# Kernel tuning notes

Hardware: AMD Instinct MI355X
Metric: run time of the kernel (lower is better)

Reference implementation:

```python
import jax, jax.numpy as jnp
import numpy as np

B, T, C = 64, 4096, 256
H = 4
HD = C // H  # head_dim = 64
EPS = 1e-5   # torch LayerNorm default


def setup_inputs() -> dict:
    key = jax.random.key(0)
    ks = jax.random.split(key, 8)
    x = jax.random.normal(ks[0], (B, T, C), dtype=jnp.float32)
    # per-head score MLP: Linear(C->HD) + Tanh + Linear(HD->1, no bias)
    W1 = jax.random.normal(ks[1], (H, C, HD), dtype=jnp.float32) * (1.0 / np.sqrt(C))
    b1 = jax.random.normal(ks[2], (H, HD), dtype=jnp.float32) * 0.02
    w2 = jax.random.normal(ks[3], (H, HD), dtype=jnp.float32) * (1.0 / np.sqrt(HD))
    # output projection Linear(H*C -> C), torch layout (out, in)
    Wo = jax.random.normal(ks[4], (C, H * C), dtype=jnp.float32) * (1.0 / np.sqrt(H * C))
    bo = jax.random.normal(ks[5], (C,), dtype=jnp.float32) * 0.02
    gamma = jnp.ones((C,), dtype=jnp.float32)
    beta = jnp.zeros((C,), dtype=jnp.float32)
    return {"x": x, "W1": W1, "b1": b1, "w2": w2, "Wo": Wo, "bo": bo,
            "gamma": gamma, "beta": beta}


def reference(x, W1, b1, w2, Wo, bo, gamma, beta):
    # All heads batched: hidden (B,H,T,HD)
    h = jnp.tanh(jnp.einsum('btc,hcd->bhtd', x, W1) + b1[None, :, None, :])
    scores = jnp.einsum('bhtd,hd->bht', h, w2)            # (B,H,T)
    weights = jax.nn.softmax(scores, axis=-1)             # softmax over T
    contexts = jnp.einsum('bht,btc->bhc', weights, x)     # (B,H,C)
    multi = contexts.reshape(B, H * C)                    # concat over heads
    out = multi @ Wo.T + bo                               # Linear(H*C->C)
    # LayerNorm over last dim (dropout is identity in eval mode)
    mu = jnp.mean(out, axis=-1, keepdims=True)
    var = jnp.mean(jnp.square(out - mu), axis=-1, keepdims=True)
    out = (out - mu) * jax.lax.rsqrt(var + EPS) * gamma + beta
    return out, weights
```

## Files before the change

### kernel.cpp

```cpp
#include <hip/hip_runtime.h>
#include <hip/hip_bf16.h>
#include <math.h>

#define B_ 64
#define T_ 4096
#define C_ 256
#define H_ 4
#define HD_ 64
#define EPS_ 1e-5f

typedef __attribute__((ext_vector_type(4))) float floatx4;
typedef __attribute__((ext_vector_type(8))) short short8;

#if __has_builtin(__builtin_amdgcn_cvt_pk_bf16_f32)
typedef __attribute__((ext_vector_type(2))) __bf16 bf16x2_t;
__device__ __forceinline__ unsigned int pack_bf16x2(float a, float b) {
    bf16x2_t v = __builtin_amdgcn_cvt_pk_bf16_f32(a, b);
    return __builtin_bit_cast(unsigned int, v);
}
#else
__device__ __forceinline__ unsigned int pack_bf16x2(float a, float b) {
    unsigned int ua = __builtin_bit_cast(unsigned int, a);
    unsigned int ub = __builtin_bit_cast(unsigned int, b);
    ua = (ua + 0x7fffu + ((ua >> 16) & 1u)) >> 16;
    ub = (ub + 0x7fffu + ((ub >> 16) & 1u)) >> 16;
    return ua | (ub << 16);
}
#endif

__device__ __forceinline__ float fast_tanh(float v) {
    float a = fabsf(v);
    float e = __expf(-2.0f * a);
#if __has_builtin(__builtin_amdgcn_rcpf)
    float r = (1.0f - e) * __builtin_amdgcn_rcpf(1.0f + e);
#else
    float r = (1.0f - e) / (1.0f + e);
#endif
    return copysignf(r, v);
}

__global__ void k0_w1frag(const float* __restrict__ W1, uint4* __restrict__ w1f) {
    int h  = blockIdx.x >> 3;
    int ks = blockIdx.x & 7;
    int nb = threadIdx.x >> 6;
    int l  = threadIdx.x & 63;
    int nl = l & 15, q = l >> 4;
    int d  = nb * 16 + nl;
    const float* src = W1 + ((long)h * C_ + ks * 32 + q * 8) * HD_ + d;
    float v[8];
    #pragma unroll
    for (int j = 0; j < 8; ++j) v[j] = src[j * HD_];
    uint4 ua;
    ua.x = pack_bf16x2(v[0], v[1]); ua.y = pack_bf16x2(v[2], v[3]);
    ua.z = pack_bf16x2(v[4], v[5]); ua.w = pack_bf16x2(v[6], v[7]);
    w1f[((long)blockIdx.x * 4 + nb) * 64 + l] = ua;
}

#define ASTRIDE 264
__global__ __launch_bounds__(256, 4)
void k1_fused(const float* __restrict__ x, const uint4* __restrict__ w1f,
              const float* __restrict__ b1, const float* __restrict__ w2,
              float* __restrict__ rawscore, float* __restrict__ ctxp,
              float* __restrict__ mS) {
    __shared__ __align__(16) unsigned short shA[64 * ASTRIDE];
    __shared__ float sS[4 * 64];
    __shared__ __align__(16) float sP4[64 * 4];

    const int tid  = threadIdx.x;
    const int lane = tid & 63;
    const int w    = tid >> 6;
    const int nl   = lane & 15;
    const int q    = lane >> 4;
    const int rowbase = blockIdx.x * 64;
    const int b       = blockIdx.x >> 6;
    const int tbase   = (blockIdx.x & 63) * 64;

    const int arow = tid >> 2;
    const int acol = (tid & 3) * 8;
    const float* aptr = x + (long)(rowbase + arow) * C_ + acol;
    #pragma unroll
    for (int kc = 0; kc < 8; ++kc) {
        const float4* ap = (const float4*)(aptr + kc * 32);
        float4 f0 = ap[0], f1 = ap[1];
        uint4 ua;
        ua.x = pack_bf16x2(f0.x, f0.y); ua.y = pack_bf16x2(f0.z, f0.w);
        ua.z = pack_bf16x2(f1.x, f1.y); ua.w = pack_bf16x2(f1.z, f1.w);
        *(uint4*)&shA[arow * ASTRIDE + kc * 32 + acol] = ua;
    }

    floatx4 acc[4][4];
    #pragma unroll
    for (int i = 0; i < 4; ++i)
        #pragma unroll
        for (int j = 0; j < 4; ++j)
            acc[i][j] = (floatx4){0.f, 0.f, 0.f, 0.f};

    const uint4* bW = w1f + (long)w * (8 * 4 * 64) + lane;

    uint4 bFa[4], bFb[4];
    #pragma unroll
    for (int nb = 0; nb < 4; ++nb) bFa[nb] = bW[nb * 64];

    __syncthreads();

    #pragma unroll
    for (int kp = 0; kp < 4; ++kp) {
        const int ks0 = 2 * kp, ks1 = 2 * kp + 1;
        #pragma unroll
        for (int nb = 0; nb < 4; ++nb) bFb[nb] = bW[(ks1 * 4 + nb) * 64];
        #pragma unroll
        for (int mb = 0; mb < 4; ++mb) {
            short8 a = *(const short8*)&shA[(mb * 16 + nl) * ASTRIDE + ks0 * 32 + q * 8];
            #pragma unroll
            for (int nb = 0; nb < 4; ++nb)
                acc[mb][nb] = __builtin_amdgcn_mfma_f32_16x16x32_bf16(
                    a, __builtin_bit_cast(short8, bFa[nb]), acc[mb][nb], 0, 0, 0);
        }
        if (kp < 3) {
            #pragma unroll
            for (int nb = 0; nb < 4; ++nb) bFa[nb] = bW[((ks0 + 2) * 4 + nb) * 64];
        }
        #pragma unroll
        for (int mb = 0; mb < 4; ++mb) {
            short8 a = *(const short8*)&shA[(mb * 16 + nl) * ASTRIDE + ks1 * 32 + q * 8];
            #pragma unroll
            for (int nb = 0; nb < 4; ++nb)
                acc[mb][nb] = __builtin_amdgcn_mfma_f32_16x16x32_bf16(
                    a, __builtin_bit_cast(short8, bFb[nb]), acc[mb][nb], 0, 0, 0);
        }
    }

    float b1v[4], w2v[4];
    #pragma unroll
    for (int nb = 0; nb < 4; ++nb) {
        int d = nb * 16 + nl;
        b1v[nb] = b1[w * HD_ + d];
        w2v[nb] = w2[w * HD_ + d];
    }
    #pragma unroll
    for (int mb = 0; mb < 4; ++mb) {
        float p[4];
        #pragma unroll
        for (int r = 0; r < 4; ++r) {
            float s = 0.f;
            #pragma unroll
            for (int nb = 0; nb < 4; ++nb)
                s += fast_tanh(acc[mb][nb][r] + b1v[nb]) * w2v[nb];
            p[r] = s;
        }
        #pragma unroll
        for (int m = 1; m < 16; m <<= 1)
            #pragma unroll
            for (int r = 0; r < 4; ++r)
                p[r] += __shfl_xor(p[r], m, 64);
        if (nl == 0) {
            #pragma unroll
            for (int r = 0; r < 4; ++r)
                sS[w * 64 + mb * 16 + q * 4 + r] = p[r];
        }
    }

    {
        float s = sS[w * 64 + lane];
        float m = s;
        #pragma unroll
        for (int off = 1; off < 64; off <<= 1)
            m = fmaxf(m, __shfl_xor(m, off, 64));
        float e = __expf(s - m);
        float Ss = e;
        #pragma unroll
        for (int off = 1; off < 64; off <<= 1)
            Ss += __shfl_xor(Ss, off, 64);
        sP4[lane * 4 + w] = e;
        rawscore[((long)(b * H_ + w)) * T_ + tbase + lane] = s;
        if (lane == 0) {
            mS[((long)blockIdx.x * H_ + w) * 2 + 0] = m;
            mS[((long)blockIdx.x * H_ + w) * 2 + 1] = Ss;
        }
    }
    __syncthreads();

    {
        float c0 = 0.f, c1 = 0.f, c2 = 0.f, c3 = 0.f;
        const float* xr = x + (long)rowbase * C_ + tid;
        const float4* pv4 = (const float4*)sP4;
        #pragma unroll 8
        for (int t = 0; t < 64; ++t) {
            float xv = xr[(long)t * C_];
            float4 pv = pv4[t];
            c0 += pv.x * xv;
            c1 += pv.y * xv;
            c2 += pv.z * xv;
            c3 += pv.w * xv;
        }
        float* o = ctxp + (long)blockIdx.x * (H_ * C_) + tid;
        o[0]   = c0;
        o[256] = c1;
        o[512] = c2;
        o[768] = c3;
    }
}

__global__ void k2_combine(const float* __restrict__ ctxp, const float* __restrict__ mS,
                           float* __restrict__ weights, float* __restrict__ multi) {
    __shared__ float sm[64], sSl[64], sc[64];
    int bh = blockIdx.x;
    int b = bh >> 2, h = bh & 3;
    int tid = threadIdx.x;
    if (tid < 64) {
        long blk = (long)b * 64 + tid;
        sm[tid]  = mS[(blk * H_ + h) * 2 + 0];
        sSl[tid] = mS[(blk * H_ + h) * 2 + 1];
    }
    __syncthreads();
    float m = -INFINITY;
    #pragma unroll 8
    for (int j = 0; j < 64; ++j) m = fmaxf(m, sm[j]);
    if (tid < 64) sc[tid] = __expf(sm[tid] - m);
    __syncthreads();
    float S = 0.f;
    #pragma unroll 8
    for (int j = 0; j < 64; ++j) S += sSl[j] * sc[j];
    float invS = 1.0f / S;

    float acc = 0.f;
    #pragma unroll 4
    for (int j = 0; j < 64; ++j)
        acc += ctxp[((long)(b * 64 + j) * H_ + h) * C_ + tid] * sc[j];
    multi[(long)b * (H_ * C_) + h * C_ + tid] = acc * invS;

    float* wr = weights + (long)bh * T_;
    #pragma unroll
    for (int i = 0; i < 16; ++i) {
        int t = tid + i * 256;
        float sv = wr[t];
        wr[t] = __expf(sv - m) * invS;
    }
}

__global__ void k4_out(const float* __restrict__ multiG, const float* __restrict__ Wo,
                       const float* __restrict__ bo, const float* __restrict__ gamma,
                       const float* __restrict__ beta, float* __restrict__ out) {
    __shared__ float multi[1024];
    __shared__ float red[256];
    int b = blockIdx.x, tid = threadIdx.x;
    {
        const float4* src = (const float4*)(multiG + (long)b * 1024);
        float4* dst = (float4*)multi;
        dst[tid] = src[tid];
    }
    __syncthreads();
    float a0 = 0.f, a1 = 0.f, a2 = 0.f, a3 = 0.f;
    const float4* wrow = (const float4*)(Wo + (long)tid * 1024);
    const float4* mv = (const float4*)multi;
    #pragma unroll 8
    for (int j4 = 0; j4 < 256; j4 += 4) {
        float4 w0 = wrow[j4],     m0 = mv[j4];
        float4 w1 = wrow[j4 + 1], m1 = mv[j4 + 1];
        float4 w2 = wrow[j4 + 2], m2 = mv[j4 + 2];
        float4 w3 = wrow[j4 + 3], m3 = mv[j4 + 3];
        a0 += m0.x * w0.x + m0.y * w0.y + m0.z * w0.z + m0.w * w0.w;
        a1 += m1.x * w1.x + m1.y * w1.y + m1.z * w1.z + m1.w * w1.w;
        a2 += m2.x * w2.x + m2.y * w2.y + m2.z * w2.z + m2.w * w2.w;
        a3 += m3.x * w3.x + m3.y * w3.y + m3.z * w3.z + m3.w * w3.w;
    }
    float acc = bo[tid] + ((a0 + a1) + (a2 + a3));
    red[tid] = acc; __syncthreads();
    for (int st = 128; st > 0; st >>= 1) {
        if (tid < st) red[tid] += red[tid + st];
        __syncthreads();
    }
    float mu = red[0] * (1.0f / 256.0f); __syncthreads();
    float dv = acc - mu;
    red[tid] = dv * dv; __syncthreads();
    for (int st = 128; st > 0; st >>= 1) {
        if (tid < st) red[tid] += red[tid + st];
        __syncthreads();
    }
    float var = red[0] * (1.0f / 256.0f);
    out[(long)b * C_ + tid] = dv * rsqrtf(var + EPS_) * gamma[tid] + beta[tid];
}

extern "C" void kernel_launch(void* const* d_in, const int* in_sizes, int n_in,
                              void* d_out, int out_size, void* d_ws, size_t ws_size,
                              hipStream_t stream) {
    const float* x     = (const float*)d_in[0];
    const float* W1    = (const float*)d_in[1];
    const float* b1    = (const float*)d_in[2];
    const float* w2    = (const float*)d_in[3];
    const float* Wo    = (const float*)d_in[4];
    const float* bo    = (const float*)d_in[5];
    const float* gamma = (const float*)d_in[6];
    const float* beta  = (const float*)d_in[7];

    float* out     = (float*)d_out;
    float* weights = out + B_ * C_;

    float* ctxp  = (float*)d_ws;
    float* mS    = ctxp + (long)4096 * H_ * C_;
    float* multi = mS + (long)4096 * H_ * 2;
    uint4* w1f   = (uint4*)(multi + B_ * H_ * C_);

    k0_w1frag <<<32, 256, 0, stream>>>(W1, w1f);
    k1_fused  <<<4096, 256, 0, stream>>>(x, w1f, b1, w2, weights, ctxp, mS);
    k2_combine<<<256, 256, 0, stream>>>(ctxp, mS, weights, multi);
    k4_out    <<<64, 256, 0, stream>>>(multi, Wo, bo, gamma, beta, out);
}
```

Baseline: 467.2 us.

## Split each head's hidden dim across two waves with 512-thread blocks

Doubles the k1 block to 8 waves. Each head's 64 hidden units are now split across two waves, and their partial scores are summed in shared memory before the softmax. The x staging and the context accumulation are also split across twice as many threads. The aim is more parallelism and latency hiding per block, at the cost of an extra barrier, idle waves during the softmax, and possibly lower occupancy per CU from the larger blocks.

```diff
diff --git a/kernel.cpp b/kernel.cpp
--- a/kernel.cpp
+++ b/kernel.cpp
@@ -57,49 +57,52 @@
 }
 
 #define ASTRIDE 264
-__global__ __launch_bounds__(256, 4)
+__global__ __launch_bounds__(512, 4)
 void k1_fused(const float* __restrict__ x, const uint4* __restrict__ w1f,
               const float* __restrict__ b1, const float* __restrict__ w2,
               float* __restrict__ rawscore, float* __restrict__ ctxp,
               float* __restrict__ mS) {
     __shared__ __align__(16) unsigned short shA[64 * ASTRIDE];
-    __shared__ float sS[4 * 64];
+    __shared__ float sS[2 * 4 * 64];
     __shared__ __align__(16) float sP4[64 * 4];
 
     const int tid  = threadIdx.x;
     const int lane = tid & 63;
-    const int w    = tid >> 6;
+    const int wid  = tid >> 6;
+    const int h    = wid >> 1;
+    const int nh   = wid & 1;
     const int nl   = lane & 15;
     const int q    = lane >> 4;
     const int rowbase = blockIdx.x * 64;
     const int b       = blockIdx.x >> 6;
     const int tbase   = (blockIdx.x & 63) * 64;
 
-    const int arow = tid >> 2;
-    const int acol = (tid & 3) * 8;
-    const float* aptr = x + (long)(rowbase + arow) * C_ + acol;
-    #pragma unroll
-    for (int kc = 0; kc < 8; ++kc) {
-        const float4* ap = (const float4*)(aptr + kc * 32);
-        float4 f0 = ap[0], f1 = ap[1];
-        uint4 ua;
-        ua.x = pack_bf16x2(f0.x, f0.y); ua.y = pack_bf16x2(f0.z, f0.w);
-        ua.z = pack_bf16x2(f1.x, f1.y); ua.w = pack_bf16x2(f1.z, f1.w);
-        *(uint4*)&shA[arow * ASTRIDE + kc * 32 + acol] = ua;
-    }
-
-    floatx4 acc[4][4];
+    {
+        const int arow = tid >> 3;
+        const int acol = (tid & 7) * 32;
+        const float4* ap = (const float4*)(x + (long)(rowbase + arow) * C_ + acol);
+        #pragma unroll
+        for (int i = 0; i < 4; ++i) {
+            float4 f0 = ap[2 * i], f1 = ap[2 * i + 1];
+            uint4 ua;
+            ua.x = pack_bf16x2(f0.x, f0.y); ua.y = pack_bf16x2(f0.z, f0.w);
+            ua.z = pack_bf16x2(f1.x, f1.y); ua.w = pack_bf16x2(f1.z, f1.w);
+            *(uint4*)&shA[arow * ASTRIDE + acol + i * 8] = ua;
+        }
+    }
+
+    floatx4 acc[4][2];
     #pragma unroll
     for (int i = 0; i < 4; ++i)
         #pragma unroll
-        for (int j = 0; j < 4; ++j)
+        for (int j = 0; j < 2; ++j)
             acc[i][j] = (floatx4){0.f, 0.f, 0.f, 0.f};
 
-    const uint4* bW = w1f + (long)w * (8 * 4 * 64) + lane;
-
-    uint4 bFa[4], bFb[4];
-    #pragma unroll
-    for (int nb = 0; nb < 4; ++nb) bFa[nb] = bW[nb * 64];
+    const uint4* bW = w1f + (long)h * (8 * 4 * 64) + lane;
+
+    uint4 bFa[2], bFb[2];
+    #pragma unroll
+    for (int nb2 = 0; nb2 < 2; ++nb2) bFa[nb2] = bW[(nh * 2 + nb2) * 64];
 
     __syncthreads();
 
@@ -107,35 +110,35 @@
     for (int kp = 0; kp < 4; ++kp) {
         const int ks0 = 2 * kp, ks1 = 2 * kp + 1;
         #pragma unroll
-        for (int nb = 0; nb < 4; ++nb) bFb[nb] = bW[(ks1 * 4 + nb) * 64];
+        for (int nb2 = 0; nb2 < 2; ++nb2) bFb[nb2] = bW[(ks1 * 4 + nh * 2 + nb2) * 64];
         #pragma unroll
         for (int mb = 0; mb < 4; ++mb) {
             short8 a = *(const short8*)&shA[(mb * 16 + nl) * ASTRIDE + ks0 * 32 + q * 8];
             #pragma unroll
-            for (int nb = 0; nb < 4; ++nb)
-                acc[mb][nb] = __builtin_amdgcn_mfma_f32_16x16x32_bf16(
-                    a, __builtin_bit_cast(short8, bFa[nb]), acc[mb][nb], 0, 0, 0);
+            for (int nb2 = 0; nb2 < 2; ++nb2)
+                acc[mb][nb2] = __builtin_amdgcn_mfma_f32_16x16x32_bf16(
+                    a, __builtin_bit_cast(short8, bFa[nb2]), acc[mb][nb2], 0, 0, 0);
         }
         if (kp < 3) {
             #pragma unroll
-            for (int nb = 0; nb < 4; ++nb) bFa[nb] = bW[((ks0 + 2) * 4 + nb) * 64];
+            for (int nb2 = 0; nb2 < 2; ++nb2) bFa[nb2] = bW[((ks0 + 2) * 4 + nh * 2 + nb2) * 64];
         }
         #pragma unroll
         for (int mb = 0; mb < 4; ++mb) {
             short8 a = *(const short8*)&shA[(mb * 16 + nl) * ASTRIDE + ks1 * 32 + q * 8];
             #pragma unroll
-            for (int nb = 0; nb < 4; ++nb)
-                acc[mb][nb] = __builtin_amdgcn_mfma_f32_16x16x32_bf16(
-                    a, __builtin_bit_cast(short8, bFb[nb]), acc[mb][nb], 0, 0, 0);
-        }
-    }
-
-    float b1v[4], w2v[4];
-    #pragma unroll
-    for (int nb = 0; nb < 4; ++nb) {
-        int d = nb * 16 + nl;
-        b1v[nb] = b1[w * HD_ + d];
-        w2v[nb] = w2[w * HD_ + d];
+            for (int nb2 = 0; nb2 < 2; ++nb2)
+                acc[mb][nb2] = __builtin_amdgcn_mfma_f32_16x16x32_bf16(
+                    a, __builtin_bit_cast(short8, bFb[nb2]), acc[mb][nb2], 0, 0, 0);
+        }
+    }
+
+    float b1v[2], w2v[2];
+    #pragma unroll
+    for (int nb2 = 0; nb2 < 2; ++nb2) {
+        int d = (nh * 2 + nb2) * 16 + nl;
+        b1v[nb2] = b1[h * HD_ + d];
+        w2v[nb2] = w2[h * HD_ + d];
     }
     #pragma unroll
     for (int mb = 0; mb < 4; ++mb) {
@@ -144,8 +147,8 @@
         for (int r = 0; r < 4; ++r) {
             float s = 0.f;
             #pragma unroll
-            for (int nb = 0; nb < 4; ++nb)
-                s += fast_tanh(acc[mb][nb][r] + b1v[nb]) * w2v[nb];
+            for (int nb2 = 0; nb2 < 2; ++nb2)
+                s += fast_tanh(acc[mb][nb2][r] + b1v[nb2]) * w2v[nb2];
             p[r] = s;
         }
         #pragma unroll
@@ -156,12 +159,14 @@
         if (nl == 0) {
             #pragma unroll
             for (int r = 0; r < 4; ++r)
-                sS[w * 64 + mb * 16 + q * 4 + r] = p[r];
-        }
-    }
-
-    {
-        float s = sS[w * 64 + lane];
+                sS[(nh * 4 + h) * 64 + mb * 16 + q * 4 + r] = p[r];
+        }
+    }
+    __syncthreads();
+
+    if (tid < 256) {
+        const int w = tid >> 6;
+        float s = sS[w * 64 + lane] + sS[(4 + w) * 64 + lane];
         float m = s;
         #pragma unroll
         for (int off = 1; off < 64; off <<= 1)
@@ -181,23 +186,21 @@
     __syncthreads();
 
     {
-        float c0 = 0.f, c1 = 0.f, c2 = 0.f, c3 = 0.f;
-        const float* xr = x + (long)rowbase * C_ + tid;
-        const float4* pv4 = (const float4*)sP4;
+        const int c  = tid & 255;
+        const int th = tid >> 8;
+        float c0 = 0.f, c1 = 0.f;
+        const float* xr = x + (long)rowbase * C_ + c;
+        const float2* pv2 = (const float2*)sP4;
         #pragma unroll 8
         for (int t = 0; t < 64; ++t) {
             float xv = xr[(long)t * C_];
-            float4 pv = pv4[t];
+            float2 pv = pv2[t * 2 + th];
             c0 += pv.x * xv;
             c1 += pv.y * xv;
-            c2 += pv.z * xv;
-            c3 += pv.w * xv;
-        }
-        float* o = ctxp + (long)blockIdx.x * (H_ * C_) + tid;
+        }
+        float* o = ctxp + (long)blockIdx.x * (H_ * C_) + th * 512 + c;
         o[0]   = c0;
         o[256] = c1;
-        o[512] = c2;
-        o[768] = c3;
     }
 }
 
@@ -302,7 +305,7 @@
     uint4* w1f   = (uint4*)(multi + B_ * H_ * C_);
 
     k0_w1frag <<<32, 256, 0, stream>>>(W1, w1f);
-    k1_fused  <<<4096, 256, 0, stream>>>(x, w1f, b1, w2, weights, ctxp, mS);
+    k1_fused  <<<4096, 512, 0, stream>>>(x, w1f, b1, w2, weights, ctxp, mS);
     k2_combine<<<256, 256, 0, stream>>>(ctxp, mS, weights, multi);
     k4_out    <<<64, 256, 0, stream>>>(multi, Wo, bo, gamma, beta, out);
 }
```

Measured after the change: 478.6 us. +2.4%, slower.

## Halve k1 row tile to 32, double block count, simplify tanh

Applied to the files above, without the earlier changes.

The fused score/context kernel now processes 32 timesteps per block instead of 64, which doubles the grid to 8192 blocks and raises the occupancy hint to 5 blocks per CU. The combine kernel is adjusted to merge 128 partial blocks per batch. The x staging load is rewritten as row-contiguous float4 reads. tanh becomes a sign-free exp2/rcp form. In exchange, each W1 fragment loaded per block now feeds half as many rows, and the partial-context buffer that k1 writes and k2 reads is twice as large.

```diff
diff --git a/kernel.cpp b/kernel.cpp
--- a/kernel.cpp
+++ b/kernel.cpp
@@ -8,6 +8,9 @@
 #define H_ 4
 #define HD_ 64
 #define EPS_ 1e-5f
+
+#define TILE_ 32
+#define NBLK_ 128
 
 typedef __attribute__((ext_vector_type(4))) float floatx4;
 typedef __attribute__((ext_vector_type(8))) short short8;
@@ -29,14 +32,17 @@
 #endif
 
 __device__ __forceinline__ float fast_tanh(float v) {
-    float a = fabsf(v);
-    float e = __expf(-2.0f * a);
+    float t = v * 2.8853900817779268f;
+#if __has_builtin(__builtin_amdgcn_exp2f)
+    float e2 = __builtin_amdgcn_exp2f(t);
+#else
+    float e2 = exp2f(t);
+#endif
 #if __has_builtin(__builtin_amdgcn_rcpf)
-    float r = (1.0f - e) * __builtin_amdgcn_rcpf(1.0f + e);
+    return fmaf(-2.0f, __builtin_amdgcn_rcpf(e2 + 1.0f), 1.0f);
 #else
-    float r = (1.0f - e) / (1.0f + e);
+    return 1.0f - 2.0f / (e2 + 1.0f);
 #endif
-    return copysignf(r, v);
 }
 
 __global__ void k0_w1frag(const float* __restrict__ W1, uint4* __restrict__ w1f) {
@@ -57,40 +63,40 @@
 }
 
 #define ASTRIDE 264
-__global__ __launch_bounds__(256, 4)
+__global__ __launch_bounds__(256, 5)
 void k1_fused(const float* __restrict__ x, const uint4* __restrict__ w1f,
               const float* __restrict__ b1, const float* __restrict__ w2,
               float* __restrict__ rawscore, float* __restrict__ ctxp,
               float* __restrict__ mS) {
-    __shared__ __align__(16) unsigned short shA[64 * ASTRIDE];
-    __shared__ float sS[4 * 64];
-    __shared__ __align__(16) float sP4[64 * 4];
+    __shared__ __align__(16) unsigned short shA[TILE_ * ASTRIDE];
+    __shared__ float sS[4 * TILE_];
+    __shared__ __align__(16) float sP4[TILE_ * 4];
 
     const int tid  = threadIdx.x;
     const int lane = tid & 63;
     const int w    = tid >> 6;
     const int nl   = lane & 15;
     const int q    = lane >> 4;
-    const int rowbase = blockIdx.x * 64;
-    const int b       = blockIdx.x >> 6;
-    const int tbase   = (blockIdx.x & 63) * 64;
-
-    const int arow = tid >> 2;
-    const int acol = (tid & 3) * 8;
-    const float* aptr = x + (long)(rowbase + arow) * C_ + acol;
-    #pragma unroll
-    for (int kc = 0; kc < 8; ++kc) {
-        const float4* ap = (const float4*)(aptr + kc * 32);
-        float4 f0 = ap[0], f1 = ap[1];
-        uint4 ua;
-        ua.x = pack_bf16x2(f0.x, f0.y); ua.y = pack_bf16x2(f0.z, f0.w);
-        ua.z = pack_bf16x2(f1.x, f1.y); ua.w = pack_bf16x2(f1.z, f1.w);
-        *(uint4*)&shA[arow * ASTRIDE + kc * 32 + acol] = ua;
-    }
-
-    floatx4 acc[4][4];
-    #pragma unroll
-    for (int i = 0; i < 4; ++i)
+    const int rowbase = blockIdx.x * TILE_;
+    const int b       = blockIdx.x >> 7;
+    const int tbase   = (blockIdx.x & 127) * TILE_;
+
+    {
+        const int r0 = w * 8;
+        const float* xp = x + (long)(rowbase + r0) * C_ + lane * 4;
+        #pragma unroll
+        for (int i = 0; i < 8; ++i) {
+            float4 f = *(const float4*)(xp + (long)i * C_);
+            uint2 u;
+            u.x = pack_bf16x2(f.x, f.y);
+            u.y = pack_bf16x2(f.z, f.w);
+            *(uint2*)&shA[(r0 + i) * ASTRIDE + lane * 4] = u;
+        }
+    }
+
+    floatx4 acc[2][4];
+    #pragma unroll
+    for (int i = 0; i < 2; ++i)
         #pragma unroll
         for (int j = 0; j < 4; ++j)
             acc[i][j] = (floatx4){0.f, 0.f, 0.f, 0.f};
@@ -109,7 +115,7 @@
         #pragma unroll
         for (int nb = 0; nb < 4; ++nb) bFb[nb] = bW[(ks1 * 4 + nb) * 64];
         #pragma unroll
-        for (int mb = 0; mb < 4; ++mb) {
+        for (int mb = 0; mb < 2; ++mb) {
             short8 a = *(const short8*)&shA[(mb * 16 + nl) * ASTRIDE + ks0 * 32 + q * 8];
             #pragma unroll
             for (int nb = 0; nb < 4; ++nb)
@@ -121,7 +127,7 @@
             for (int nb = 0; nb < 4; ++nb) bFa[nb] = bW[((ks0 + 2) * 4 + nb) * 64];
         }
         #pragma unroll
-        for (int mb = 0; mb < 4; ++mb) {
+        for (int mb = 0; mb < 2; ++mb) {
             short8 a = *(const short8*)&shA[(mb * 16 + nl) * ASTRIDE + ks1 * 32 + q * 8];
             #pragma unroll
             for (int nb = 0; nb < 4; ++nb)
@@ -138,7 +144,7 @@
         w2v[nb] = w2[w * HD_ + d];
     }
     #pragma unroll
-    for (int mb = 0; mb < 4; ++mb) {
+    for (int mb = 0; mb < 2; ++mb) {
         float p[4];
         #pragma unroll
         for (int r = 0; r < 4; ++r) {
@@ -156,26 +162,29 @@
         if (nl == 0) {
             #pragma unroll
             for (int r = 0; r < 4; ++r)
-                sS[w * 64 + mb * 16 + q * 4 + r] = p[r];
-        }
-    }
-
-    {
-        float s = sS[w * 64 + lane];
+                sS[w * TILE_ + mb * 16 + q * 4 + r] = p[r];
+        }
+    }
+    __syncthreads();
+
+    if (tid < 128) {
+        const int wh = tid >> 5;
+        const int tl = tid & 31;
+        float s = sS[wh * TILE_ + tl];
         float m = s;
         #pragma unroll
-        for (int off = 1; off < 64; off <<= 1)
-            m = fmaxf(m, __shfl_xor(m, off, 64));
+        for (int off = 1; off < 32; off <<= 1)
+            m = fmaxf(m, __shfl_xor(m, off, 32));
         float e = __expf(s - m);
         float Ss = e;
         #pragma unroll
-        for (int off = 1; off < 64; off <<= 1)
-            Ss += __shfl_xor(Ss, off, 64);
-        sP4[lane * 4 + w] = e;
-        rawscore[((long)(b * H_ + w)) * T_ + tbase + lane] = s;
-        if (lane == 0) {
-            mS[((long)blockIdx.x * H_ + w) * 2 + 0] = m;
-            mS[((long)blockIdx.x * H_ + w) * 2 + 1] = Ss;
+        for (int off = 1; off < 32; off <<= 1)
+            Ss += __shfl_xor(Ss, off, 32);
+        sP4[tl * 4 + wh] = e;
+        rawscore[((long)(b * H_ + wh)) * T_ + tbase + tl] = s;
+        if (tl == 0) {
+            mS[((long)blockIdx.x * H_ + wh) * 2 + 0] = m;
+            mS[((long)blockIdx.x * H_ + wh) * 2 + 1] = Ss;
         }
     }
     __syncthreads();
@@ -185,7 +194,7 @@
         const float* xr = x + (long)rowbase * C_ + tid;
         const float4* pv4 = (const float4*)sP4;
         #pragma unroll 8
-        for (int t = 0; t < 64; ++t) {
+        for (int t = 0; t < TILE_; ++t) {
             float xv = xr[(long)t * C_];
             float4 pv = pv4[t];
             c0 += pv.x * xv;
@@ -203,30 +212,30 @@
 
 __global__ void k2_combine(const float* __restrict__ ctxp, const float* __restrict__ mS,
                            float* __restrict__ weights, float* __restrict__ multi) {
-    __shared__ float sm[64], sSl[64], sc[64];
+    __shared__ float sm[NBLK_], sSl[NBLK_], sc[NBLK_];
     int bh = blockIdx.x;
     int b = bh >> 2, h = bh & 3;
     int tid = threadIdx.x;
-    if (tid < 64) {
-        long blk = (long)b * 64 + tid;
+    if (tid < NBLK_) {
+        long blk = (long)b * NBLK_ + tid;
         sm[tid]  = mS[(blk * H_ + h) * 2 + 0];
         sSl[tid] = mS[(blk * H_ + h) * 2 + 1];
     }
     __syncthreads();
     float m = -INFINITY;
     #pragma unroll 8
-    for (int j = 0; j < 64; ++j) m = fmaxf(m, sm[j]);
-    if (tid < 64) sc[tid] = __expf(sm[tid] - m);
+    for (int j = 0; j < NBLK_; ++j) m = fmaxf(m, sm[j]);
+    if (tid < NBLK_) sc[tid] = __expf(sm[tid] - m);
     __syncthreads();
     float S = 0.f;
     #pragma unroll 8
-    for (int j = 0; j < 64; ++j) S += sSl[j] * sc[j];
+    for (int j = 0; j < NBLK_; ++j) S += sSl[j] * sc[j];
     float invS = 1.0f / S;
 
     float acc = 0.f;
     #pragma unroll 4
-    for (int j = 0; j < 64; ++j)
-        acc += ctxp[((long)(b * 64 + j) * H_ + h) * C_ + tid] * sc[j];
+    for (int j = 0; j < NBLK_; ++j)
+        acc += ctxp[((long)(b * NBLK_ + j) * H_ + h) * C_ + tid] * sc[j];
     multi[(long)b * (H_ * C_) + h * C_ + tid] = acc * invS;
 
     float* wr = weights + (long)bh * T_;
@@ -296,13 +305,14 @@
     float* out     = (float*)d_out;
     float* weights = out + B_ * C_;
 
+    const long NB = (long)B_ * NBLK_;
     float* ctxp  = (float*)d_ws;
-    float* mS    = ctxp + (long)4096 * H_ * C_;
-    float* multi = mS + (long)4096 * H_ * 2;
+    float* mS    = ctxp + NB * (H_ * C_);
+    float* multi = mS + NB * H_ * 2;
     uint4* w1f   = (uint4*)(multi + B_ * H_ * C_);
 
     k0_w1frag <<<32, 256, 0, stream>>>(W1, w1f);
-    k1_fused  <<<4096, 256, 0, stream>>>(x, w1f, b1, w2, weights, ctxp, mS);
+    k1_fused  <<<NB, 256, 0, stream>>>(x, w1f, b1, w2, weights, ctxp, mS);
     k2_combine<<<256, 256, 0, stream>>>(ctxp, mS, weights, multi);
     k4_out    <<<64, 256, 0, stream>>>(multi, Wo, bo, gamma, beta, out);
 }
```

After: 475.6 us. No clear change (+1.8%).

## Split combine and output stages into wider-parallel kernels, simplify tanh

Applied to the files above, without the earlier changes.

Splits the combine kernel so context reduction uses 1024 threads across four slices, and moves the softmax weight normalization into a separate float4-vectorized kernel over 512 blocks. The output projection is split into a 1024-block kernel using wave-level shuffle reductions, followed by a small LayerNorm kernel. fast_tanh is rewritten as 1-2/(exp2(2x*log2e)+1), dropping the abs/copysign. This adds two launches and small workspace buffers, and aims to fix the under-parallelized tail kernels.

```diff
diff --git a/kernel.cpp b/kernel.cpp
--- a/kernel.cpp
+++ b/kernel.cpp
@@ -8,6 +8,9 @@
 #define H_ 4
 #define HD_ 64
 #define EPS_ 1e-5f
+
+#define TILE_ 64
+#define NBLK_ 64
 
 typedef __attribute__((ext_vector_type(4))) float floatx4;
 typedef __attribute__((ext_vector_type(8))) short short8;
@@ -29,14 +32,17 @@
 #endif
 
 __device__ __forceinline__ float fast_tanh(float v) {
-    float a = fabsf(v);
-    float e = __expf(-2.0f * a);
+    float t = v * 2.8853900817779268f;
+#if __has_builtin(__builtin_amdgcn_exp2f)
+    float e2 = __builtin_amdgcn_exp2f(t);
+#else
+    float e2 = exp2f(t);
+#endif
 #if __has_builtin(__builtin_amdgcn_rcpf)
-    float r = (1.0f - e) * __builtin_amdgcn_rcpf(1.0f + e);
+    return fmaf(-2.0f, __builtin_amdgcn_rcpf(e2 + 1.0f), 1.0f);
 #else
-    float r = (1.0f - e) / (1.0f + e);
+    return 1.0f - 2.0f / (e2 + 1.0f);
 #endif
-    return copysignf(r, v);
 }
 
 __global__ void k0_w1frag(const float* __restrict__ W1, uint4* __restrict__ w1f) {
@@ -62,18 +68,18 @@
               const float* __restrict__ b1, const float* __restrict__ w2,
               float* __restrict__ rawscore, float* __restrict__ ctxp,
               float* __restrict__ mS) {
-    __shared__ __align__(16) unsigned short shA[64 * ASTRIDE];
-    __shared__ float sS[4 * 64];
-    __shared__ __align__(16) float sP4[64 * 4];
+    __shared__ __align__(16) unsigned short shA[TILE_ * ASTRIDE];
+    __shared__ float sS[4 * TILE_];
+    __shared__ __align__(16) float sP4[TILE_ * 4];
 
     const int tid  = threadIdx.x;
     const int lane = tid & 63;
     const int w    = tid >> 6;
     const int nl   = lane & 15;
     const int q    = lane >> 4;
-    const int rowbase = blockIdx.x * 64;
+    const int rowbase = blockIdx.x * TILE_;
     const int b       = blockIdx.x >> 6;
-    const int tbase   = (blockIdx.x & 63) * 64;
+    const int tbase   = (blockIdx.x & 63) * TILE_;
 
     const int arow = tid >> 2;
     const int acol = (tid & 3) * 8;
@@ -156,12 +162,12 @@
         if (nl == 0) {
             #pragma unroll
             for (int r = 0; r < 4; ++r)
-                sS[w * 64 + mb * 16 + q * 4 + r] = p[r];
+                sS[w * TILE_ + mb * 16 + q * 4 + r] = p[r];
         }
     }
 
     {
-        float s = sS[w * 64 + lane];
+        float s = sS[w * TILE_ + lane];
         float m = s;
         #pragma unroll
         for (int off = 1; off < 64; off <<= 1)
@@ -185,7 +191,7 @@
         const float* xr = x + (long)rowbase * C_ + tid;
         const float4* pv4 = (const float4*)sP4;
         #pragma unroll 8
-        for (int t = 0; t < 64; ++t) {
+        for (int t = 0; t < TILE_; ++t) {
             float xv = xr[(long)t * C_];
             float4 pv = pv4[t];
             c0 += pv.x * xv;
@@ -201,70 +207,102 @@
     }
 }
 
-__global__ void k2_combine(const float* __restrict__ ctxp, const float* __restrict__ mS,
-                           float* __restrict__ weights, float* __restrict__ multi) {
-    __shared__ float sm[64], sSl[64], sc[64];
+__global__ __launch_bounds__(1024)
+void k2_combine(const float* __restrict__ ctxp, const float* __restrict__ mS,
+                float* __restrict__ gms, float* __restrict__ multi) {
+    __shared__ float sm[NBLK_], sSl[NBLK_];
+    __shared__ float red[4][256];
     int bh = blockIdx.x;
     int b = bh >> 2, h = bh & 3;
     int tid = threadIdx.x;
-    if (tid < 64) {
-        long blk = (long)b * 64 + tid;
+    int c  = tid & 255;
+    int js = tid >> 8;
+    if (tid < NBLK_) {
+        long blk = (long)b * NBLK_ + tid;
         sm[tid]  = mS[(blk * H_ + h) * 2 + 0];
         sSl[tid] = mS[(blk * H_ + h) * 2 + 1];
     }
     __syncthreads();
     float m = -INFINITY;
     #pragma unroll 8
-    for (int j = 0; j < 64; ++j) m = fmaxf(m, sm[j]);
-    if (tid < 64) sc[tid] = __expf(sm[tid] - m);
-    __syncthreads();
+    for (int j = 0; j < NBLK_; ++j) m = fmaxf(m, sm[j]);
     float S = 0.f;
     #pragma unroll 8
-    for (int j = 0; j < 64; ++j) S += sSl[j] * sc[j];
+    for (int j = 0; j < NBLK_; ++j) S += sSl[j] * __expf(sm[j] - m);
     float invS = 1.0f / S;
+    if (tid == 0) { gms[bh * 2 + 0] = m; gms[bh * 2 + 1] = invS; }
 
     float acc = 0.f;
-    #pragma unroll 4
-    for (int j = 0; j < 64; ++j)
-        acc += ctxp[((long)(b * 64 + j) * H_ + h) * C_ + tid] * sc[j];
-    multi[(long)b * (H_ * C_) + h * C_ + tid] = acc * invS;
-
-    float* wr = weights + (long)bh * T_;
-    #pragma unroll
-    for (int i = 0; i < 16; ++i) {
-        int t = tid + i * 256;
-        float sv = wr[t];
-        wr[t] = __expf(sv - m) * invS;
-    }
-}
-
-__global__ void k4_out(const float* __restrict__ multiG, const float* __restrict__ Wo,
-                       const float* __restrict__ bo, const float* __restrict__ gamma,
+    #pragma unroll
+    for (int jj = 0; jj < NBLK_ / 4; ++jj) {
+        int j = js * (NBLK_ / 4) + jj;
+        acc += ctxp[((long)(b * NBLK_ + j) * H_ + h) * C_ + c] * __expf(sm[j] - m);
+    }
+    red[js][c] = acc;
+    __syncthreads();
+    if (js == 0)
+        multi[(long)b * (H_ * C_) + h * C_ + c] =
+            (red[0][c] + red[1][c] + red[2][c] + red[3][c]) * invS;
+}
+
+__global__ void k3_weights(const float* __restrict__ gms, float* __restrict__ weights) {
+    int bh = blockIdx.x >> 1, half = blockIdx.x & 1;
+    float m = gms[bh * 2 + 0], invS = gms[bh * 2 + 1];
+    float4* wr = (float4*)(weights + (long)bh * T_ + half * 2048);
+    int tid = threadIdx.x;
+    #pragma unroll
+    for (int i = 0; i < 2; ++i) {
+        float4 v = wr[tid + i * 256];
+        v.x = __expf(v.x - m) * invS;
+        v.y = __expf(v.y - m) * invS;
+        v.z = __expf(v.z - m) * invS;
+        v.w = __expf(v.w - m) * invS;
+        wr[tid + i * 256] = v;
+    }
+}
+
+__global__ __launch_bounds__(256)
+void k4a_proj(const float* __restrict__ multiG, const float* __restrict__ Wo,
+              const float* __restrict__ bo, float* __restrict__ outraw) {
+    __shared__ __align__(16) float multi[1024];
+    int b = blockIdx.x >> 4, cs = blockIdx.x & 15;
+    int tid = threadIdx.x, w = tid >> 6, l = tid & 63;
+    ((float4*)multi)[tid] = ((const float4*)(multiG + (long)b * 1024))[tid];
+    __syncthreads();
+    float a[4];
+    #pragma unroll
+    for (int cc = 0; cc < 4; ++cc) {
+        int c = cs * 16 + w * 4 + cc;
+        const float4* wrow = (const float4*)(Wo + (long)c * 1024);
+        const float4* mv = (const float4*)multi;
+        float s = 0.f;
+        #pragma unroll
+        for (int k = 0; k < 4; ++k) {
+            float4 wv = wrow[k * 64 + l];
+            float4 m4 = mv[k * 64 + l];
+            s += wv.x * m4.x + wv.y * m4.y + wv.z * m4.z + wv.w * m4.w;
+        }
+        a[cc] = s;
+    }
+    #pragma unroll
+    for (int off = 1; off < 64; off <<= 1)
+        #pragma unroll
+        for (int cc = 0; cc < 4; ++cc)
+            a[cc] += __shfl_xor(a[cc], off, 64);
+    if (l == 0) {
+        #pragma unroll
+        for (int cc = 0; cc < 4; ++cc) {
+            int c = cs * 16 + w * 4 + cc;
+            outraw[(long)b * C_ + c] = a[cc] + bo[c];
+        }
+    }
+}
+
+__global__ void k4b_ln(const float* __restrict__ outraw, const float* __restrict__ gamma,
                        const float* __restrict__ beta, float* __restrict__ out) {
-    __shared__ float multi[1024];
     __shared__ float red[256];
     int b = blockIdx.x, tid = threadIdx.x;
-    {
-        const float4* src = (const float4*)(multiG + (long)b * 1024);
-        float4* dst = (float4*)multi;
-        dst[tid] = src[tid];
-    }
-    __syncthreads();
-    float a0 = 0.f, a1 = 0.f, a2 = 0.f, a3 = 0.f;
-    const float4* wrow = (const float4*)(Wo + (long)tid * 1024);
-    const float4* mv = (const float4*)multi;
-    #pragma unroll 8
-    for (int j4 = 0; j4 < 256; j4 += 4) {
-        float4 w0 = wrow[j4],     m0 = mv[j4];
-        float4 w1 = wrow[j4 + 1], m1 = mv[j4 + 1];
-        float4 w2 = wrow[j4 + 2], m2 = mv[j4 + 2];
-        float4 w3 = wrow[j4 + 3], m3 = mv[j4 + 3];
-        a0 += m0.x * w0.x + m0.y * w0.y + m0.z * w0.z + m0.w * w0.w;
-        a1 += m1.x * w1.x + m1.y * w1.y + m1.z * w1.z + m1.w * w1.w;
-        a2 += m2.x * w2.x + m2.y * w2.y + m2.z * w2.z + m2.w * w2.w;
-        a3 += m3.x * w3.x + m3.y * w3.y + m3.z * w3.z + m3.w * w3.w;
-    }
-    float acc = bo[tid] + ((a0 + a1) + (a2 + a3));
+    float acc = outraw[(long)b * C_ + tid];
     red[tid] = acc; __syncthreads();
     for (int st = 128; st > 0; st >>= 1) {
         if (tid < st) red[tid] += red[tid + st];
@@ -296,13 +334,18 @@
     float* out     = (float*)d_out;
     float* weights = out + B_ * C_;
 
-    float* ctxp  = (float*)d_ws;
-    float* mS    = ctxp + (long)4096 * H_ * C_;
-    float* multi = mS + (long)4096 * H_ * 2;
-    uint4* w1f   = (uint4*)(multi + B_ * H_ * C_);
+    const long NB = (long)B_ * NBLK_;
+    float* ctxp   = (float*)d_ws;
+    float* mS     = ctxp + NB * (H_ * C_);
+    float* multi  = mS + NB * H_ * 2;
+    uint4* w1f    = (uint4*)(multi + B_ * H_ * C_);
+    float* gms    = (float*)w1f + 32768;
+    float* outraw = gms + 512;
 
     k0_w1frag <<<32, 256, 0, stream>>>(W1, w1f);
-    k1_fused  <<<4096, 256, 0, stream>>>(x, w1f, b1, w2, weights, ctxp, mS);
-    k2_combine<<<256, 256, 0, stream>>>(ctxp, mS, weights, multi);
-    k4_out    <<<64, 256, 0, stream>>>(multi, Wo, bo, gamma, beta, out);
-}
+    k1_fused  <<<NB, 256, 0, stream>>>(x, w1f, b1, w2, weights, ctxp, mS);
+    k2_combine<<<256, 1024, 0, stream>>>(ctxp, mS, gms, multi);
+    k3_weights<<<512, 256, 0, stream>>>(gms, weights);
+    k4a_proj  <<<1024, 256, 0, stream>>>(multi, Wo, bo, outraw);
+    k4b_ln    <<<64, 256, 0, stream>>>(outraw, gamma, beta, out);
+}
```

New measurement: 423.5 us. -9.4%, faster.
